# Kernel optimization log

Measured on AMD Instinct MI355X. Metric: run time of the kernel, lower is better.

## Reference

```python
import jax, jax.numpy as jnp
import numpy as np

B, L, D, E = 64, 256, 2048, 1024
WIN = 3
NEG = -1e18


def setup_inputs() -> dict:
    key = jax.random.key(0)
    ks = jax.random.split(key, 8)
    clip_ft = jax.random.normal(ks[0], (B, L, D), dtype=jnp.float32)
    clip_lens = jax.random.randint(ks[1], (B,), 3, L + 1).astype(jnp.int32)
    s = 1.0 / np.sqrt(D)
    w_mot_wei = jax.random.uniform(ks[2], (D,), minval=-s, maxval=s)
    b_mot_wei = jnp.zeros((), jnp.float32)
    w_mot_fc = jax.random.uniform(ks[3], (D, E), minval=-s, maxval=s)
    b_mot_fc = jnp.zeros((E,), jnp.float32)
    w_app_fc = jax.random.uniform(ks[4], (D, E), minval=-s, maxval=s)
    b_app_fc = jnp.zeros((E,), jnp.float32)
    se = 1.0 / np.sqrt(E)
    w_pool = jax.random.uniform(ks[5], (E,), minval=-se, maxval=se)
    b_pool = jnp.zeros((), jnp.float32)
    return {"clip_ft": clip_ft, "clip_lens": clip_lens,
            "w_mot_wei": w_mot_wei, "b_mot_wei": b_mot_wei,
            "w_mot_fc": w_mot_fc, "b_mot_fc": b_mot_fc,
            "w_app_fc": w_app_fc, "b_app_fc": b_app_fc,
            "w_pool": w_pool, "b_pool": b_pool}


def _gelu(x):
    return jax.nn.gelu(x, approximate=False)  # torch nn.GELU default (erf)


def reference(clip_ft, clip_lens, w_mot_wei, b_mot_wei, w_mot_fc, b_mot_fc,
              w_app_fc, b_app_fc, w_pool, b_pool):
    b, l, d = clip_ft.shape
    pos = jnp.arange(l)
    pad = pos[None, :] >= clip_lens[:, None]                      # True = pad
    mot_scores = clip_ft @ w_mot_wei + b_mot_wei                  # (B, L)
    attn_scores = jnp.where(pad, NEG, mot_scores)
    # sliding window of size 3 (vectorized replacement of the python loop)
    lw = l - WIN + 1                                              # L - 2
    win_ft = jnp.stack([clip_ft[:, i:i + lw] for i in range(WIN)], axis=2)   # (B, L-2, 3, D)
    win_sc = jnp.stack([attn_scores[:, i:i + lw] for i in range(WIN)], axis=2)  # (B, L-2, 3)
    a = jax.nn.softmax(win_sc, axis=2)
    vid_clip = jnp.einsum('blw,blwd->bld', a, win_ft)             # (B, L-2, D)
    motion = _gelu(vid_clip @ w_mot_fc + b_mot_fc)                # (B, L-2, E)
    appearance = _gelu(clip_ft @ w_app_fc + b_app_fc)             # (B, L, E)
    # masked-softmax attention pooling (motion uses lens-2, appearance uses lens)
    s_mot = _gelu(motion @ w_pool + b_pool)                       # (B, L-2)
    pad_mot = jnp.arange(lw)[None, :] >= (clip_lens - 2)[:, None]
    a_mot = jax.nn.softmax(jnp.where(pad_mot, NEG, s_mot), axis=1)
    mot_pooled = jnp.einsum('bl,ble->be', a_mot, motion)          # (B, E)
    s_app = _gelu(appearance @ w_pool + b_pool)                   # (B, L)
    a_app = jax.nn.softmax(jnp.where(pad, NEG, s_app), axis=1)
    app_pooled = jnp.einsum('bl,ble->be', a_app, appearance)      # (B, E)
    return jnp.concatenate([mot_pooled, app_pooled], axis=-1)     # (B, 2E)
```

## Files before the change

### kernel.cpp

```cpp
#include <hip/hip_runtime.h>
#include <cstdint>

#define NEGF (-1e18f)
#define GK 2048
#define GN 1024

typedef __attribute__((ext_vector_type(8))) short short8;
typedef __attribute__((ext_vector_type(4))) float f32x4;
typedef __attribute__((ext_vector_type(4))) unsigned short us4;
typedef __attribute__((ext_vector_type(8))) unsigned short us8;

__device__ __forceinline__ unsigned short f2bf(float f) {
    unsigned int u = __float_as_uint(f);
    u += 0x7FFFu + ((u >> 16) & 1u);
    return (unsigned short)(u >> 16);
}
__device__ __forceinline__ float bf2f(unsigned short h) {
    return __uint_as_float(((unsigned int)h) << 16);
}
__device__ __forceinline__ float gelu_erf(float x) {
    return 0.5f * x * (1.0f + erff(x * 0.70710678118654752f));
}
__device__ __forceinline__ float gelu_fast(float x) {
    const float y = 1.5957691216057308f * (x + 0.044715f * x * x * x);
    const float t = 1.0f - 2.0f / (__expf(y) + 1.0f);
    return 0.5f * x * (1.0f + t);
}
__device__ __forceinline__ void async_copy16(const void* g, void* l) {
    __builtin_amdgcn_global_load_lds(
        (const __attribute__((address_space(1))) unsigned int*)g,
        (__attribute__((address_space(3))) unsigned int*)l,
        16, 0, 0);
}

__global__ __launch_bounds__(64) void scan_kernel(const int* __restrict__ lens,
                                                  int* __restrict__ bases) {
    const int lane = threadIdx.x;
    const int L = lens[lane];
    int sm_ = L - 2, sa_ = L;
    const int vm = sm_, va = sa_;
    #pragma unroll
    for (int off = 1; off < 64; off <<= 1) {
        const int tm = __shfl_up(sm_, off);
        const int ta = __shfl_up(sa_, off);
        if (lane >= off) { sm_ += tm; sa_ += ta; }
    }
    bases[lane] = sm_ - vm;
    bases[65 + lane] = sa_ - va;
    if (lane == 63) { bases[64] = sm_; bases[129] = sa_; }
}

__global__ __launch_bounds__(256) void wtrans2_kernel(const float* __restrict__ wmot,
                                                      const float* __restrict__ wapp,
                                                      unsigned short* __restrict__ wmotT,
                                                      unsigned short* __restrict__ wappT) {
    const int which = blockIdx.x >> 10;
    const float* w = which ? wapp : wmot;
    unsigned short* wT = which ? wappT : wmotT;
    const int idx = (blockIdx.x & 1023) * 256 + threadIdx.x;
    const int n = idx & 1023;
    const int k0 = (idx >> 10) << 3;
    us8 o;
    #pragma unroll
    for (int j = 0; j < 8; ++j) o[j] = f2bf(w[(size_t)(k0 + j) * 1024 + n]);
    *(us8*)(wT + (size_t)n * 2048 + k0) = o;
}

__global__ __launch_bounds__(256) void prep2_kernel(const float* __restrict__ clip_ft,
                                                    const int* __restrict__ lens,
                                                    const int* __restrict__ bases,
                                                    const float* __restrict__ w_mot_wei,
                                                    const float* __restrict__ bsc,
                                                    unsigned short* __restrict__ app,
                                                    unsigned short* __restrict__ vid) {
    __shared__ float sm2[2][4];
    const int b = blockIdx.x >> 3;
    const int c = blockIdx.x & 7;
    const int len = lens[b];
    const int l0 = c * 32;
    if (l0 >= len) return;
    const int bm = bases[b], ba = bases[65 + b];
    const int t = threadIdx.x;
    const int lane = t & 63, wv = t >> 6;
    const int d0 = t * 8;
    const float bias = bsc[0];
    const float* base = clip_ft + ((size_t)b * 256) * 2048 + d0;
    float wm[8];
    {
        f32x4 u = *(const f32x4*)(w_mot_wei + d0);
        f32x4 v = *(const f32x4*)(w_mot_wei + d0 + 4);
        #pragma unroll
        for (int j = 0; j < 4; ++j) { wm[j] = u[j]; wm[4 + j] = v[j]; }
    }
    float x0[8], x1[8], cur[8];
    float sc0 = NEGF, sc1 = NEGF, sc2 = NEGF;
    for (int i = 0; i < 34; ++i) {
        const int l = l0 + i;
        if (l < 256) {
            const f32x4* p = (const f32x4*)(base + (size_t)l * 2048);
            f32x4 u = p[0], v = p[1];
            #pragma unroll
            for (int j = 0; j < 4; ++j) { cur[j] = u[j]; cur[4 + j] = v[j]; }
            if (i < 32 && l < len) {
                us8 o;
                #pragma unroll
                for (int j = 0; j < 8; ++j) o[j] = f2bf(cur[j]);
                *(us8*)(app + ((size_t)(ba + l)) * 2048 + d0) = o;
            }
            float p8 = cur[0]*wm[0] + cur[1]*wm[1] + cur[2]*wm[2] + cur[3]*wm[3]
                     + cur[4]*wm[4] + cur[5]*wm[5] + cur[6]*wm[6] + cur[7]*wm[7];
            #pragma unroll
            for (int off = 32; off; off >>= 1) p8 += __shfl_xor(p8, off);
            if (lane == 0) sm2[i & 1][wv] = p8;
        }
        __syncthreads();
        if (l < 256) {
            float s = (sm2[i & 1][0] + sm2[i & 1][1]) + (sm2[i & 1][2] + sm2[i & 1][3]) + bias;
            sc2 = (l >= len) ? NEGF : s;
        }
        if (i >= 2) {
            const int lw = l - 2;
            if (lw < len - 2) {
                const float mx = fmaxf(sc0, fmaxf(sc1, sc2));
                const float e0 = expf(sc0 - mx), e1 = expf(sc1 - mx), e2 = expf(sc2 - mx);
                const float inv = 1.0f / (e0 + e1 + e2);
                const float a0 = e0 * inv, a1 = e1 * inv, a2 = e2 * inv;
                us8 o;
                #pragma unroll
                for (int j = 0; j < 8; ++j) o[j] = f2bf(a0 * x0[j] + a1 * x1[j] + a2 * cur[j]);
                *(us8*)(vid + ((size_t)(bm + lw)) * 2048 + d0) = o;
            }
        }
        #pragma unroll
        for (int j = 0; j < 8; ++j) { x0[j] = x1[j]; x1[j] = cur[j]; }
        sc0 = sc1; sc1 = sc2;
    }
}

__global__ __launch_bounds__(512, 4) void gemm3q_kernel(
        const unsigned short* __restrict__ Avid, const unsigned short* __restrict__ Aapp,
        const unsigned short* __restrict__ Bmot, const unsigned short* __restrict__ Bapp,
        const float* __restrict__ bmot, const float* __restrict__ bapp,
        const float* __restrict__ w_pool, const int* __restrict__ bases,
        unsigned short* __restrict__ Cmot, unsigned short* __restrict__ Capp,
        float* __restrict__ pspart) {
    __shared__ __align__(16) unsigned short lds_[3 * 12288];
    const int bid = blockIdx.x;
    const int virt = (bid & 7) * 128 + (bid >> 3);
    const int which = virt >> 9;
    const int rem = virt & 511;
    const int ntile = rem & 3;
    const int mt_idx = rem >> 2;
    const int mtile = (mt_idx & 31) * 4 + (mt_idx >> 5);
    const int row0 = mtile * 128, col0 = ntile * 256;
    const int total = bases[which ? 129 : 64];
    if (row0 >= total) return;
    const unsigned short* A  = which ? Aapp : Avid;
    const unsigned short* Bt = which ? Bapp : Bmot;
    const float* bias        = which ? bapp : bmot;
    unsigned short* C        = which ? Capp : Cmot;
    const int t = threadIdx.x, lane = t & 63, wave = t >> 6;
    const int wm = wave >> 2, wn = wave & 3;
    const int lr = lane & 15, sl = lane >> 4;

    const int srow = t >> 2;
    const int sk16 = (t & 3) ^ ((srow >> 1) & 3);
    const unsigned short* gA  = A  + (size_t)(row0 + srow) * GK + sk16 * 8;
    const unsigned short* gB0 = Bt + (size_t)(col0 + srow) * GK + sk16 * 8;
    const unsigned short* gB1 = Bt + (size_t)(col0 + srow + 128) * GK + sk16 * 8;
    const int wbase = wave << 9;

#define STAGE(d, kt) do { \
    async_copy16(gA  + (kt) * 32, lds_ + (d) * 12288 +        wbase); \
    async_copy16(gB0 + (kt) * 32, lds_ + (d) * 12288 + 4096 + wbase); \
    async_copy16(gB1 + (kt) * 32, lds_ + (d) * 12288 + 8192 + wbase); } while (0)

#define KSTEP(CUR) do { \
    const unsigned short* lb = lds_ + (CUR) * 12288; \
    short8 aF[4], bF[4]; \
    _Pragma("unroll") \
    for (int m = 0; m < 4; ++m) { \
        const int r = wm * 64 + m * 16 + lr; \
        aF[m] = *(const short8*)(lb + r * 32 + ((sl ^ ((r >> 1) & 3)) << 3)); \
    } \
    _Pragma("unroll") \
    for (int n = 0; n < 4; ++n) { \
        const int cc = wn * 64 + n * 16 + lr; \
        bF[n] = *(const short8*)(lb + 4096 + cc * 32 + ((sl ^ ((cc >> 1) & 3)) << 3)); \
    } \
    _Pragma("unroll") \
    for (int m = 0; m < 4; ++m) \
        _Pragma("unroll") \
        for (int n = 0; n < 4; ++n) \
            acc[m][n] = __builtin_amdgcn_mfma_f32_16x16x32_bf16(aF[m], bF[n], acc[m][n], 0, 0, 0); \
    } while (0)

    f32x4 acc[4][4] = {};
    STAGE(0, 0);
    STAGE(1, 1);

    int cur = 0, stg = 2;
    #pragma unroll 3
    for (int kt = 0; kt < 62; ++kt) {
        asm volatile("s_waitcnt vmcnt(3)" ::: "memory");
        __builtin_amdgcn_s_barrier();
        __builtin_amdgcn_sched_barrier(0);
        STAGE(stg, kt + 2);
        KSTEP(cur);
        cur = (cur == 2) ? 0 : cur + 1;
        stg = (stg == 2) ? 0 : stg + 1;
    }
    asm volatile("s_waitcnt vmcnt(3)" ::: "memory");
    __builtin_amdgcn_s_barrier();
    __builtin_amdgcn_sched_barrier(0);
    KSTEP(cur);
    cur = (cur == 2) ? 0 : cur + 1;
    asm volatile("s_waitcnt vmcnt(0)" ::: "memory");
    __builtin_amdgcn_s_barrier();
    __builtin_amdgcn_sched_barrier(0);
    KSTEP(cur);
#undef STAGE
#undef KSTEP

    float wp[4], bz[4];
    #pragma unroll
    for (int n = 0; n < 4; ++n) {
        const int col = col0 + wn * 64 + n * 16 + lr;
        wp[n] = w_pool[col];
        bz[n] = bias[col];
    }
    const int strip = ntile * 4 + wn;
    #pragma unroll
    for (int m = 0; m < 4; ++m) {
        #pragma unroll
        for (int i = 0; i < 4; ++i) {
            const int row = row0 + wm * 64 + m * 16 + sl * 4 + i;
            float pr = 0.f;
            #pragma unroll
            for (int n = 0; n < 4; ++n) {
                const int col = col0 + wn * 64 + n * 16 + lr;
                const float g = gelu_fast(acc[m][n][i] + bz[n]);
                pr += g * wp[n];
                C[(size_t)row * GN + col] = f2bf(g);
            }
            #pragma unroll
            for (int off = 8; off; off >>= 1) pr += __shfl_xor(pr, off);
            if (lr == 0) pspart[((size_t)which * 16384 + row) * 16 + strip] = pr;
        }
    }
}

__global__ __launch_bounds__(256) void pool2_kernel(const unsigned short* __restrict__ motion,
                                                    const unsigned short* __restrict__ appearance,
                                                    const float* __restrict__ pspart,
                                                    const int* __restrict__ lens,
                                                    const int* __restrict__ bases,
                                                    const float* __restrict__ b_pool,
                                                    float* __restrict__ out) {
    __shared__ float sm[256];
    __shared__ float red[8];
    const int which = blockIdx.x & 1;
    const int b = blockIdx.x >> 1;
    const int base = which ? bases[65 + b] : bases[b];
    const unsigned short* mat = (which ? appearance : motion) + (size_t)base * 1024;
    const int valid = which ? lens[b] : lens[b] - 2;
    const int t = threadIdx.x, lane = t & 63, wv = t >> 6;
    float v = NEGF;
    if (t < valid) {
        const float* pp = pspart + ((size_t)which * 16384 + base + t) * 16;
        float s = 0.f;
        #pragma unroll
        for (int j = 0; j < 16; ++j) s += pp[j];
        v = gelu_erf(s + b_pool[0]);
    }
    float mx = v;
    #pragma unroll
    for (int off = 32; off; off >>= 1) mx = fmaxf(mx, __shfl_xor(mx, off));
    if (lane == 0) red[wv] = mx;
    __syncthreads();
    mx = fmaxf(fmaxf(red[0], red[1]), fmaxf(red[2], red[3]));
    const float e = expf(v - mx);
    float s = e;
    #pragma unroll
    for (int off = 32; off; off >>= 1) s += __shfl_xor(s, off);
    if (lane == 0) red[4 + wv] = s;
    __syncthreads();
    s = red[4] + red[5] + red[6] + red[7];
    sm[t] = e / s;
    __syncthreads();
    const int col0 = t * 4;
    float a0 = 0.f, a1 = 0.f, a2 = 0.f, a3 = 0.f;
    for (int l = 0; l < valid; ++l) {
        const float al = sm[l];
        us4 hv = *(const us4*)(mat + (size_t)l * 1024 + col0);
        a0 += al * bf2f(hv[0]);
        a1 += al * bf2f(hv[1]);
        a2 += al * bf2f(hv[2]);
        a3 += al * bf2f(hv[3]);
    }
    float* o = out + (size_t)b * 2048 + which * 1024 + col0;
    o[0] = a0; o[1] = a1; o[2] = a2; o[3] = a3;
}

extern "C" void kernel_launch(void* const* d_in, const int* in_sizes, int n_in,
                              void* d_out, int out_size, void* d_ws, size_t ws_size,
                              hipStream_t stream) {
    const float* clip_ft   = (const float*)d_in[0];
    const int*   clip_lens = (const int*)d_in[1];
    const float* w_mot_wei = (const float*)d_in[2];
    const float* b_mot_wei = (const float*)d_in[3];
    const float* w_mot_fc  = (const float*)d_in[4];
    const float* b_mot_fc  = (const float*)d_in[5];
    const float* w_app_fc  = (const float*)d_in[6];
    const float* b_app_fc  = (const float*)d_in[7];
    const float* w_pool    = (const float*)d_in[8];
    const float* b_pool    = (const float*)d_in[9];
    float* out = (float*)d_out;

    char* ws = (char*)d_ws;
    size_t off = 0;
    auto carve = [&](size_t bytes) { void* p = ws + off; off += (bytes + 255) & ~(size_t)255; return p; };
    int*            bases  = (int*)carve((size_t)130 * 4);
    float*          pspart = (float*)carve((size_t)2 * 16384 * 16 * 4);
    unsigned short* wmotT  = (unsigned short*)carve((size_t)1024 * 2048 * 2);
    unsigned short* wappT  = (unsigned short*)carve((size_t)1024 * 2048 * 2);
    unsigned short* appb   = (unsigned short*)carve((size_t)64 * 256 * 2048 * 2);
    unsigned short* vidb   = (unsigned short*)carve((size_t)64 * 256 * 2048 * 2);
    unsigned short* motion = (unsigned short*)carve((size_t)64 * 256 * 1024 * 2);
    unsigned short* appear = (unsigned short*)carve((size_t)64 * 256 * 1024 * 2);
    (void)ws_size; (void)in_sizes; (void)n_in; (void)out_size;

    scan_kernel<<<1, 64, 0, stream>>>(clip_lens, bases);
    wtrans2_kernel<<<2048, 256, 0, stream>>>(w_mot_fc, w_app_fc, wmotT, wappT);
    prep2_kernel<<<512, 256, 0, stream>>>(clip_ft, clip_lens, bases, w_mot_wei, b_mot_wei,
                                          appb, vidb);
    gemm3q_kernel<<<1024, 512, 0, stream>>>(vidb, appb, wmotT, wappT,
                                            b_mot_fc, b_app_fc, w_pool, bases,
                                            motion, appear, pspart);
    pool2_kernel<<<128, 256, 0, stream>>>(motion, appear, pspart, clip_lens, bases, b_pool, out);
}
```

Baseline: 166.2 us.

## Fold scan into weight transpose, skip padded rows in prep, split pooling columns

```diff
diff --git a/kernel.cpp b/kernel.cpp
--- a/kernel.cpp
+++ b/kernel.cpp
@@ -33,27 +33,30 @@
         16, 0, 0);
 }
 
-__global__ __launch_bounds__(64) void scan_kernel(const int* __restrict__ lens,
-                                                  int* __restrict__ bases) {
-    const int lane = threadIdx.x;
-    const int L = lens[lane];
-    int sm_ = L - 2, sa_ = L;
-    const int vm = sm_, va = sa_;
-    #pragma unroll
-    for (int off = 1; off < 64; off <<= 1) {
-        const int tm = __shfl_up(sm_, off);
-        const int ta = __shfl_up(sa_, off);
-        if (lane >= off) { sm_ += tm; sa_ += ta; }
-    }
-    bases[lane] = sm_ - vm;
-    bases[65 + lane] = sa_ - va;
-    if (lane == 63) { bases[64] = sm_; bases[129] = sa_; }
-}
-
 __global__ __launch_bounds__(256) void wtrans2_kernel(const float* __restrict__ wmot,
                                                       const float* __restrict__ wapp,
+                                                      const int* __restrict__ lens,
                                                       unsigned short* __restrict__ wmotT,
-                                                      unsigned short* __restrict__ wappT) {
+                                                      unsigned short* __restrict__ wappT,
+                                                      int* __restrict__ bases) {
+    if (blockIdx.x == 2048) {
+        const int lane = threadIdx.x;
+        if (lane < 64) {
+            const int L = lens[lane];
+            int sm_ = L - 2, sa_ = L;
+            const int vm = sm_, va = sa_;
+            #pragma unroll
+            for (int off = 1; off < 64; off <<= 1) {
+                const int tm = __shfl_up(sm_, off);
+                const int ta = __shfl_up(sa_, off);
+                if (lane >= off) { sm_ += tm; sa_ += ta; }
+            }
+            bases[lane] = sm_ - vm;
+            bases[65 + lane] = sa_ - va;
+            if (lane == 63) { bases[64] = sm_; bases[129] = sa_; }
+        }
+        return;
+    }
     const int which = blockIdx.x >> 10;
     const float* w = which ? wapp : wmot;
     unsigned short* wT = which ? wappT : wmotT;
@@ -96,12 +99,13 @@
     float sc0 = NEGF, sc1 = NEGF, sc2 = NEGF;
     for (int i = 0; i < 34; ++i) {
         const int l = l0 + i;
-        if (l < 256) {
+        const bool live = (l < len);
+        if (live) {
             const f32x4* p = (const f32x4*)(base + (size_t)l * 2048);
             f32x4 u = p[0], v = p[1];
             #pragma unroll
             for (int j = 0; j < 4; ++j) { cur[j] = u[j]; cur[4 + j] = v[j]; }
-            if (i < 32 && l < len) {
+            if (i < 32) {
                 us8 o;
                 #pragma unroll
                 for (int j = 0; j < 8; ++j) o[j] = f2bf(cur[j]);
@@ -114,10 +118,8 @@
             if (lane == 0) sm2[i & 1][wv] = p8;
         }
         __syncthreads();
-        if (l < 256) {
-            float s = (sm2[i & 1][0] + sm2[i & 1][1]) + (sm2[i & 1][2] + sm2[i & 1][3]) + bias;
-            sc2 = (l >= len) ? NEGF : s;
-        }
+        sc2 = live ? (sm2[i & 1][0] + sm2[i & 1][1]) + (sm2[i & 1][2] + sm2[i & 1][3]) + bias
+                   : NEGF;
         if (i >= 2) {
             const int lw = l - 2;
             if (lw < len - 2) {
@@ -260,7 +262,8 @@
     __shared__ float sm[256];
     __shared__ float red[8];
     const int which = blockIdx.x & 1;
-    const int b = blockIdx.x >> 1;
+    const int half = (blockIdx.x >> 1) & 1;
+    const int b = blockIdx.x >> 2;
     const int base = which ? bases[65 + b] : bases[b];
     const unsigned short* mat = (which ? appearance : motion) + (size_t)base * 1024;
     const int valid = which ? lens[b] : lens[b] - 2;
@@ -288,18 +291,16 @@
     s = red[4] + red[5] + red[6] + red[7];
     sm[t] = e / s;
     __syncthreads();
-    const int col0 = t * 4;
-    float a0 = 0.f, a1 = 0.f, a2 = 0.f, a3 = 0.f;
+    const int col0 = half * 512 + t * 2;
+    float a0 = 0.f, a1 = 0.f;
     for (int l = 0; l < valid; ++l) {
         const float al = sm[l];
-        us4 hv = *(const us4*)(mat + (size_t)l * 1024 + col0);
-        a0 += al * bf2f(hv[0]);
-        a1 += al * bf2f(hv[1]);
-        a2 += al * bf2f(hv[2]);
-        a3 += al * bf2f(hv[3]);
+        const unsigned int hv = *(const unsigned int*)(mat + (size_t)l * 1024 + col0);
+        a0 += al * bf2f((unsigned short)(hv & 0xFFFF));
+        a1 += al * bf2f((unsigned short)(hv >> 16));
     }
     float* o = out + (size_t)b * 2048 + which * 1024 + col0;
-    o[0] = a0; o[1] = a1; o[2] = a2; o[3] = a3;
+    o[0] = a0; o[1] = a1;
 }
 
 extern "C" void kernel_launch(void* const* d_in, const int* in_sizes, int n_in,
@@ -330,12 +331,12 @@
     unsigned short* appear = (unsigned short*)carve((size_t)64 * 256 * 1024 * 2);
     (void)ws_size; (void)in_sizes; (void)n_in; (void)out_size;
 
-    scan_kernel<<<1, 64, 0, stream>>>(clip_lens, bases);
-    wtrans2_kernel<<<2048, 256, 0, stream>>>(w_mot_fc, w_app_fc, wmotT, wappT);
+    wtrans2_kernel<<<2049, 256, 0, stream>>>(w_mot_fc, w_app_fc, clip_lens,
+                                             wmotT, wappT, bases);
     prep2_kernel<<<512, 256, 0, stream>>>(clip_ft, clip_lens, bases, w_mot_wei, b_mot_wei,
                                           appb, vidb);
     gemm3q_kernel<<<1024, 512, 0, stream>>>(vidb, appb, wmotT, wappT,
                                             b_mot_fc, b_app_fc, w_pool, bases,
                                             motion, appear, pspart);
-    pool2_kernel<<<128, 256, 0, stream>>>(motion, appear, pspart, clip_lens, bases, b_pool, out);
-}
+    pool2_kernel<<<256, 256, 0, stream>>>(motion, appear, pspart, clip_lens, bases, b_pool, out);
+}
```

Result: faster. 158.4 us (-4.7%).
